# Kernel optimization log

Measured on AMD Instinct MI355X. Metric: run time of the kernel, lower is better.

Reference implementation:

```python
import jax, jax.numpy as jnp
import numpy as np

# ---- fixed sizes ----
N_IN = 100_000          # total inner nodes
NODES_PER_INNER = 50    # nodes per inner graph
N_OUT = N_IN // NODES_PER_INNER          # 2000 outer nodes (= num inner graphs)
NODES_PER_OUTER = 125   # outer nodes per outer graph
B = N_OUT // NODES_PER_OUTER             # 16 graphs in the batch
DEG = 8
E_IN = N_IN * DEG        # 800_000 inner edges
E_OUT = N_OUT * DEG      # 16_000 outer edges
IN_FEATS = 64
OUT_FEATS = 64
H = 128                  # h_feats = [128]*6
NUM_CLASSES = 10


def _rand_edges(key, n_graphs, nodes_per_graph, edges_per_graph):
    """Random edges that stay inside each graph of a batched graph."""
    k1, k2 = jax.random.split(key)
    src_l = jax.random.randint(k1, (n_graphs, edges_per_graph), 0, nodes_per_graph)
    dst_l = jax.random.randint(k2, (n_graphs, edges_per_graph), 0, nodes_per_graph)
    off = (jnp.arange(n_graphs) * nodes_per_graph)[:, None]
    return ((src_l + off).reshape(-1).astype(jnp.int32),
            (dst_l + off).reshape(-1).astype(jnp.int32))


def setup_inputs() -> dict:
    key = jax.random.key(0)
    ks = jax.random.split(key, 24)
    inner_src, inner_dst = _rand_edges(ks[0], N_OUT, NODES_PER_INNER, E_IN // N_OUT)
    outer_src, outer_dst = _rand_edges(ks[1], B, NODES_PER_OUTER, E_OUT // B)

    def w(k, fan_in, fan_out):
        return jax.random.normal(k, (fan_in, fan_out), jnp.float32) * (1.0 / np.sqrt(fan_in))

    inp = {
        "in_layer_feat": jax.random.normal(ks[2], (N_IN, IN_FEATS), jnp.float32),
        "out_layer_feat": jax.random.normal(ks[3], (N_OUT, OUT_FEATS), jnp.float32),
        "inner_ew": jax.random.uniform(ks[4], (E_IN,), jnp.float32) + 0.5,
        "outer_ew": jax.random.uniform(ks[5], (E_OUT,), jnp.float32) + 0.5,
        "W1": w(ks[6], IN_FEATS, H),        "b1": jnp.zeros((H,), jnp.float32),
        "W2": w(ks[7], H, H),               "b2": jnp.zeros((H,), jnp.float32),
        "W3": w(ks[8], OUT_FEATS + H, H),   "b3": jnp.zeros((H,), jnp.float32),
        "W4": w(ks[9], H, H),               "b4": jnp.zeros((H,), jnp.float32),
        "W5": w(ks[10], H, H),              "b5": jnp.zeros((H,), jnp.float32),
        "W6": w(ks[11], H, H),              "b6": jnp.zeros((H,), jnp.float32),
        "Wc": w(ks[12], H, NUM_CLASSES),    "bc": jnp.zeros((NUM_CLASSES,), jnp.float32),
        "inner_src": inner_src, "inner_dst": inner_dst,
        "outer_src": outer_src, "outer_dst": outer_dst,
        "inner_node_graph": (jnp.arange(N_IN) // NODES_PER_INNER).astype(jnp.int32),
        "outer_node_graph": (jnp.arange(N_OUT) // NODES_PER_OUTER).astype(jnp.int32),
    }
    return inp


def graph_conv(src, dst, ew, x, W, b, n_nodes):
    """DGL GraphConv, norm='both', weighted aggregation, zero-in-degree allowed."""
    ones = jnp.ones(src.shape[0], x.dtype)
    deg_out = jnp.clip(jax.ops.segment_sum(ones, src, num_segments=n_nodes), 1.0)
    deg_in = jnp.clip(jax.ops.segment_sum(ones, dst, num_segments=n_nodes), 1.0)
    xs = x * jax.lax.rsqrt(deg_out)[:, None]                      # src normalization
    msg = xs[src] * ew[:, None]                                   # u_mul_e
    agg = jax.ops.segment_sum(msg, dst, num_segments=n_nodes)     # copy_e -> sum
    agg = agg * jax.lax.rsqrt(deg_in)[:, None]                    # dst normalization
    return agg @ W + b


def mean_nodes(h, node_graph, n_graphs, nodes_per_graph):
    return jax.ops.segment_sum(h, node_graph, num_segments=n_graphs) / nodes_per_graph


def reference(in_layer_feat, out_layer_feat, inner_ew, outer_ew,
              W1, b1, W2, b2, W3, b3, W4, b4, W5, b5, W6, b6, Wc, bc,
              inner_src, inner_dst, outer_src, outer_dst,
              inner_node_graph, outer_node_graph):
    # inner-graph message passing
    h = jax.nn.relu(graph_conv(inner_src, inner_dst, inner_ew, in_layer_feat, W1, b1, N_IN))
    h = jax.nn.relu(graph_conv(inner_src, inner_dst, inner_ew, h, W2, b2, N_IN))
    reduced = mean_nodes(h, inner_node_graph, N_OUT, float(NODES_PER_INNER))  # [N_OUT, H]
    merged = jnp.concatenate([out_layer_feat, reduced], axis=-1)              # [N_OUT, OUT_FEATS+H]
    # outer-graph message passing
    h = jax.nn.relu(graph_conv(outer_src, outer_dst, outer_ew, merged, W3, b3, N_OUT))
    h = jax.nn.relu(graph_conv(outer_src, outer_dst, outer_ew, h, W4, b4, N_OUT))
    h = jax.nn.relu(graph_conv(outer_src, outer_dst, outer_ew, h, W5, b5, N_OUT))
    h = jax.nn.relu(graph_conv(outer_src, outer_dst, outer_ew, h, W6, b6, N_OUT))
    hg = mean_nodes(h, outer_node_graph, B, float(NODES_PER_OUTER))           # [B, H]
    return hg @ Wc + bc                                                       # [B, NUM_CLASSES]
```

## Files before the change

kernel.cpp:

```cpp
#include <hip/hip_runtime.h>

#define NPI 50
#define EPI 400
#define NPO 125
#define EPO 1000
#define N_IN 100000
#define N_OUT 2000
#define NB 16
#define NC 10

typedef _Float16 half_t;
typedef _Float16 f16x8 __attribute__((ext_vector_type(8)));
typedef float f32x4 __attribute__((ext_vector_type(4)));

#define MFMA(a, b, c) __builtin_amdgcn_mfma_f32_16x16x32_f16(a, b, c, 0, 0, 0)

__device__ __forceinline__ f16x8 lds_ld8(const half_t* base, int row, int k, int strideB) {
    return *(const f16x8*)((const char*)base + row * strideB + ((k * 2) ^ ((row & 7) << 4)));
}
__device__ __forceinline__ void lds_st1(half_t* base, int row, int col, int strideB, float v) {
    *(half_t*)((char*)base + row * strideB + ((col * 2) ^ ((row & 7) << 4))) = (half_t)v;
}
__device__ __forceinline__ void lds_st1h(half_t* base, int row, int col, int strideB, half_t v) {
    *(half_t*)((char*)base + row * strideB + ((col * 2) ^ ((row & 7) << 4))) = v;
}
__device__ __forceinline__ void lds_st8(half_t* base, int row, int k, int strideB, f16x8 v) {
    *(f16x8*)((char*)base + row * strideB + ((k * 2) ^ ((row & 7) << 4))) = v;
}
__device__ __forceinline__ f16x8 scr_ld8(const half_t* base, int row, int k) {
    return *(const f16x8*)((const char*)base + row * 64 + ((k * 2) ^ ((row & 3) << 4)));
}
__device__ __forceinline__ void scr_st1(half_t* base, int row, int col, float v) {
    *(half_t*)((char*)base + row * 64 + ((col * 2) ^ ((row & 3) << 4))) = (half_t)v;
}

__global__ __launch_bounds__(256) void k_pre(
    const float* __restrict__ W1, const float* __restrict__ W2,
    const float* __restrict__ W3, const float* __restrict__ W4,
    const float* __restrict__ W5, const float* __restrict__ W6,
    half_t* __restrict__ WT1, half_t* __restrict__ WT2,
    half_t* __restrict__ WT3, half_t* __restrict__ WT4,
    half_t* __restrict__ WT5, half_t* __restrict__ WT6,
    const float* __restrict__ ew, const int* __restrict__ esrc,
    const int* __restrict__ edst, half_t* __restrict__ Aout)
{
    __shared__ float Af[NPO * NPO];
    __shared__ int cO[NPO], cI[NPO];
    __shared__ float rso[NPO], rsi[NPO];
    const int t = threadIdx.x;

    if (blockIdx.x < 384) {
        int i = blockIdx.x * 256 + t;
        const float* src; half_t* dst; int K;
        if      (i < 8192)  { src = W1; dst = WT1; K = 64; }
        else if (i < 24576) { src = W2; dst = WT2; K = 128; i -= 8192; }
        else if (i < 49152) { src = W3; dst = WT3; K = 192; i -= 24576; }
        else if (i < 65536) { src = W4; dst = WT4; K = 128; i -= 49152; }
        else if (i < 81920) { src = W5; dst = WT5; K = 128; i -= 65536; }
        else                { src = W6; dst = WT6; K = 128; i -= 81920; }
        int c = i & 127, k = i >> 7;
        dst[c * K + k] = (half_t)src[k * 128 + c];
        return;
    }

    const int g = blockIdx.x - 384;
    const int nb = g * NPO, eb = g * EPO;
    for (int i = t; i < NPO * NPO; i += 256) Af[i] = 0.f;
    if (t < NPO) { cO[t] = 0; cI[t] = 0; }
    __syncthreads();
    for (int e = t; e < EPO; e += 256) {
        int s = esrc[eb + e] - nb, d = edst[eb + e] - nb;
        atomicAdd(&Af[d * NPO + s], ew[eb + e]);
        atomicAdd(&cO[s], 1); atomicAdd(&cI[d], 1);
    }
    __syncthreads();
    if (t < NPO) {
        rso[t] = rsqrtf((float)max(cO[t], 1));
        rsi[t] = rsqrtf((float)max(cI[t], 1));
    }
    __syncthreads();
    for (int i = t; i < 128 * 16; i += 256) {
        int d = i >> 4, s0 = (i & 15) * 8;
        f16x8 v;
        #pragma unroll
        for (int j = 0; j < 8; j++) {
            int s = s0 + j;
            float x = (d < NPO && s < NPO) ? Af[d * NPO + s] * rsi[d] * rso[s] : 0.f;
            v[j] = (half_t)x;
        }
        *(f16x8*)&Aout[(size_t)g * 16384 + d * 128 + s0] = v;
    }
}

__global__ __launch_bounds__(256, 7) void k_inner(
    const float* __restrict__ X, const float* __restrict__ outfeat,
    const float* __restrict__ ew, const int* __restrict__ esrc,
    const int* __restrict__ edst,
    const half_t* __restrict__ WT1, const float* __restrict__ b1,
    const half_t* __restrict__ WT2, const float* __restrict__ b2,
    half_t* __restrict__ merged)
{
    __shared__ alignas(16) char smem[21504];
    half_t* R2  = (half_t*)smem;
    float*  Af  = (float*)smem;
    half_t* scr = (half_t*)(smem + 16384);
    float*  pool= (float*)(smem + 20480);
    int*    cO  = (int*)(smem + 20992);
    int*    cI  = (int*)(smem + 21248);

    const int g = blockIdx.x, t = threadIdx.x;
    const int w = t >> 6, l = t & 63, lr = l & 15, lk = l >> 4;
    const int nb = g * NPI, eb = g * EPI;
    half_t* scrw = scr + w * 512;

    float ofv = (t < 64) ? outfeat[(size_t)g * 64 + t] : 0.f;
    int s0e, d0e; float w0e;
    { int e = eb + t; s0e = esrc[e] - nb; d0e = edst[e] - nb; w0e = ew[e]; }
    int s1e = 0, d1e = 0; float w1e = 0.f;
    const bool e1v = (t + 256 < EPI);
    if (e1v) { int e = eb + t + 256; s1e = esrc[e] - nb; d1e = edst[e] - nb; w1e = ew[e]; }
    const int srow = t >> 2, qc = t & 3;
    float4 xr0 = {0,0,0,0}, xr1 = xr0, xr2 = xr0, xr3 = xr0;
    if (srow < NPI) {
        const float* xp = &X[(size_t)(nb + srow) * 64 + qc * 16];
        xr0 = *(const float4*)(xp + 0);
        xr1 = *(const float4*)(xp + 4);
        xr2 = *(const float4*)(xp + 8);
        xr3 = *(const float4*)(xp + 12);
    }

    if (t < 64) { cO[t] = 0; cI[t] = 0; }
    if (t >= 64 && t < 192) pool[t - 64] = 0.f;
    for (int i = t; i < 4096; i += 256) Af[i] = 0.f;
    __syncthreads();

    atomicAdd(&Af[d0e * 64 + (s0e ^ ((d0e & 7) << 2))], w0e);
    atomicAdd(&cO[s0e], 1); atomicAdd(&cI[d0e], 1);
    if (e1v) {
        atomicAdd(&Af[d1e * 64 + (s1e ^ ((d1e & 7) << 2))], w1e);
        atomicAdd(&cO[s1e], 1); atomicAdd(&cI[d1e], 1);
    }
    __syncthreads();

    f16x8 afr[2];
    {
        const int r = w * 16 + lr;
        const int sw = (r & 7) << 2;
        const float rsi_l = rsqrtf((float)max(cI[r], 1));
        #pragma unroll
        for (int ks = 0; ks < 2; ks++) {
            const int c0 = ks * 32 + lk * 8;
            f32x4 v0 = *(const f32x4*)&Af[r * 64 + (c0 ^ sw)];
            f32x4 v1 = *(const f32x4*)&Af[r * 64 + ((c0 + 4) ^ sw)];
            f16x8 fr;
            #pragma unroll
            for (int j = 0; j < 4; j++)
                fr[j] = (half_t)(v0[j] * rsi_l * rsqrtf((float)max(cO[c0 + j], 1)));
            #pragma unroll
            for (int j = 0; j < 4; j++)
                fr[4 + j] = (half_t)(v1[j] * rsi_l * rsqrtf((float)max(cO[c0 + 4 + j], 1)));
            afr[ks] = fr;
        }
    }
    __syncthreads();

    {
        float xv[16] = {xr0.x,xr0.y,xr0.z,xr0.w, xr1.x,xr1.y,xr1.z,xr1.w,
                        xr2.x,xr2.y,xr2.z,xr2.w, xr3.x,xr3.y,xr3.z,xr3.w};
        #pragma unroll
        for (int i = 0; i < 16; i++) lds_st1(R2, qc * 16 + i, srow, 128, xv[i]);
    }
    __syncthreads();

    f32x4 hacc[8] = {};
    #pragma unroll
    for (int kf = 0; kf < 2; kf++) {
        #pragma unroll
        for (int j = 0; j < 2; j++) {
            const int ft = kf * 2 + j;
            f32x4 tacc = {};
            #pragma unroll
            for (int ks = 0; ks < 2; ks++) {
                f16x8 b = lds_ld8(R2, ft * 16 + lr, ks * 32 + lk * 8, 128);
                tacc = MFMA(afr[ks], b, tacc);
            }
            #pragma unroll
            for (int q = 0; q < 4; q++) scr_st1(scrw, lk * 4 + q, j * 16 + lr, tacc[q]);
        }
        f16x8 a1 = scr_ld8(scrw, lr, lk * 8);
        #pragma unroll
        for (int nt = 0; nt < 8; nt++) {
            f16x8 b = *(const f16x8*)&WT1[(nt * 16 + lr) * 64 + kf * 32 + lk * 8];
            hacc[nt] = MFMA(a1, b, hacc[nt]);
        }
    }
    __syncthreads();
    #pragma unroll
    for (int nt = 0; nt < 8; nt++) {
        int c = nt * 16 + lr;
        float bb = b1[c];
        #pragma unroll
        for (int q = 0; q < 4; q++)
            lds_st1(R2, c, w * 16 + lk * 4 + q, 128, fmaxf(hacc[nt][q] + bb, 0.f));
    }
    __syncthreads();

    f32x4 h2[8] = {};
    #pragma unroll
    for (int kf = 0; kf < 4; kf++) {
        #pragma unroll
        for (int j = 0; j < 2; j++) {
            const int ft = kf * 2 + j;
            f32x4 tacc = {};
            #pragma unroll
            for (int ks = 0; ks < 2; ks++) {
                f16x8 b = lds_ld8(R2, ft * 16 + lr, ks * 32 + lk * 8, 128);
                tacc = MFMA(afr[ks], b, tacc);
            }
            #pragma unroll
            for (int q = 0; q < 4; q++) scr_st1(scrw, lk * 4 + q, j * 16 + lr, tacc[q]);
        }
        f16x8 a1 = scr_ld8(scrw, lr, lk * 8);
        #pragma unroll
        for (int nt = 0; nt < 8; nt++) {
            f16x8 b = *(const f16x8*)&WT2[(nt * 16 + lr) * 128 + kf * 32 + lk * 8];
            h2[nt] = MFMA(a1, b, h2[nt]);
        }
    }
    #pragma unroll
    for (int nt = 0; nt < 8; nt++) {
        int c = nt * 16 + lr;
        float bb = b2[c];
        float ps = 0.f;
        #pragma unroll
        for (int q = 0; q < 4; q++) {
            int m = w * 16 + lk * 4 + q;
            float v = fmaxf(h2[nt][q] + bb, 0.f);
            ps += (m < NPI) ? v : 0.f;
        }
        ps += __shfl_xor(ps, 16);
        ps += __shfl_xor(ps, 32);
        if (lk == 0) atomicAdd(&pool[c], ps);
    }
    __syncthreads();
    if (t < 64) merged[(size_t)g * 192 + t] = (half_t)ofv;
    else if (t < 192) merged[(size_t)g * 192 + t] = (half_t)(pool[t - 64] * (1.f / NPI));
}

template <int FIN, bool STAGE, bool LAST>
__device__ __forceinline__ void outer_layer(
    const half_t* AgL, const half_t* __restrict__ mg,
    const half_t* __restrict__ WT, const float* __restrict__ bias,
    half_t* bufP, half_t* bufQ, float* pool,
    int w, int lr, int lk, int t)
{
    f32x4 hacc[8] = {};
    constexpr int NCH = FIN / 64;
    #pragma unroll
    for (int ch = 0; ch < NCH; ch++) {
        if constexpr (STAGE) {
            __syncthreads();
            for (int i = t; i < 1024; i += 512) {
                int s = i >> 3, fo = (i & 7) * 8;
                f16x8 hv = {};
                if (s < NPO) hv = *(const f16x8*)&mg[(size_t)s * 192 + ch * 64 + fo];
                #pragma unroll
                for (int j = 0; j < 8; j++) lds_st1h(bufP, fo + j, s, 256, hv[j]);
            }
            __syncthreads();
        }
        const int rb = STAGE ? 0 : ch * 64;
        f32x4 tacc[4] = {};
        #pragma unroll
        for (int ks = 0; ks < 4; ks++) {
            f16x8 a = lds_ld8(AgL, w * 16 + lr, ks * 32 + lk * 8, 256);
            #pragma unroll
            for (int nt = 0; nt < 4; nt++) {
                f16x8 b = lds_ld8(bufP, rb + nt * 16 + lr, ks * 32 + lk * 8, 256);
                tacc[nt] = MFMA(a, b, tacc[nt]);
            }
        }
        #pragma unroll
        for (int nt = 0; nt < 4; nt++)
            #pragma unroll
            for (int q = 0; q < 4; q++)
                lds_st1(bufQ, w * 16 + lk * 4 + q, nt * 16 + lr, 128, tacc[nt][q]);
        #pragma unroll
        for (int ks2 = 0; ks2 < 2; ks2++) {
            f16x8 a1 = lds_ld8(bufQ, w * 16 + lr, ks2 * 32 + lk * 8, 128);
            #pragma unroll
            for (int nt = 0; nt < 8; nt++) {
                f16x8 b = *(const f16x8*)&WT[(nt * 16 + lr) * FIN + ch * 64 + ks2 * 32 + lk * 8];
                hacc[nt] = MFMA(a1, b, hacc[nt]);
            }
        }
    }
    __syncthreads();
    if constexpr (!LAST) {
        #pragma unroll
        for (int nt = 0; nt < 8; nt++) {
            int c = nt * 16 + lr;
            float bb = bias[c];
            #pragma unroll
            for (int q = 0; q < 4; q++)
                lds_st1(bufP, c, w * 16 + lk * 4 + q, 256, fmaxf(hacc[nt][q] + bb, 0.f));
        }
        __syncthreads();
    } else {
        #pragma unroll
        for (int nt = 0; nt < 8; nt++) {
            int c = nt * 16 + lr;
            float bb = bias[c];
            float ps = 0.f;
            #pragma unroll
            for (int q = 0; q < 4; q++) {
                int d = w * 16 + lk * 4 + q;
                float v = fmaxf(hacc[nt][q] + bb, 0.f);
                ps += (d < NPO) ? v : 0.f;
            }
            ps += __shfl_xor(ps, 16);
            ps += __shfl_xor(ps, 32);
            if (lk == 0) atomicAdd(&pool[c], ps);
        }
        __syncthreads();
    }
}

__global__ __launch_bounds__(512) void k_outer(
    const half_t* __restrict__ Aout, const half_t* __restrict__ merged,
    const half_t* __restrict__ WT3, const float* __restrict__ b3,
    const half_t* __restrict__ WT4, const float* __restrict__ b4,
    const half_t* __restrict__ WT5, const float* __restrict__ b5,
    const half_t* __restrict__ WT6, const float* __restrict__ b6,
    const float* __restrict__ Wc, const float* __restrict__ bc,
    float* __restrict__ out)
{
    __shared__ alignas(16) char smem[82432];
    half_t* AgL  = (half_t*)smem;
    half_t* bufP = (half_t*)(smem + 32768);
    half_t* bufQ = (half_t*)(smem + 65536);
    float*  pool = (float*)(smem + 81920);

    const int g = blockIdx.x, t = threadIdx.x;
    const int w = t >> 6, l = t & 63, lr = l & 15, lk = l >> 4;
    const half_t* mg = merged + (size_t)g * NPO * 192;

    for (int i = t; i < 2048; i += 512) {
        int row = i >> 4, k0 = (i & 15) * 8;
        f16x8 v = *(const f16x8*)&Aout[(size_t)g * 16384 + row * 128 + k0];
        lds_st8(AgL, row, k0, 256, v);
    }
    if (t < 128) pool[t] = 0.f;
    __syncthreads();

    outer_layer<192, true,  false>(AgL, mg, WT3, b3, bufP, bufQ, pool, w, lr, lk, t);
    outer_layer<128, false, false>(AgL, nullptr, WT4, b4, bufP, bufQ, pool, w, lr, lk, t);
    outer_layer<128, false, false>(AgL, nullptr, WT5, b5, bufP, bufQ, pool, w, lr, lk, t);
    outer_layer<128, false, true >(AgL, nullptr, WT6, b6, bufP, bufQ, pool, w, lr, lk, t);

    if (t < NC) {
        float acc = bc[t];
        for (int k = 0; k < 128; k++)
            acc = fmaf(pool[k] * (1.f / NPO), Wc[k * NC + t], acc);
        out[g * NC + t] = acc;
    }
}

extern "C" void kernel_launch(void* const* d_in, const int* in_sizes, int n_in,
                              void* d_out, int out_size, void* d_ws, size_t ws_size,
                              hipStream_t stream)
{
    const float* X       = (const float*)d_in[0];
    const float* outfeat = (const float*)d_in[1];
    const float* iew     = (const float*)d_in[2];
    const float* oew     = (const float*)d_in[3];
    const float* W1 = (const float*)d_in[4];  const float* b1 = (const float*)d_in[5];
    const float* W2 = (const float*)d_in[6];  const float* b2 = (const float*)d_in[7];
    const float* W3 = (const float*)d_in[8];  const float* b3 = (const float*)d_in[9];
    const float* W4 = (const float*)d_in[10]; const float* b4 = (const float*)d_in[11];
    const float* W5 = (const float*)d_in[12]; const float* b5 = (const float*)d_in[13];
    const float* W6 = (const float*)d_in[14]; const float* b6 = (const float*)d_in[15];
    const float* Wc = (const float*)d_in[16]; const float* bc = (const float*)d_in[17];
    const int* isrc = (const int*)d_in[18];   const int* idst = (const int*)d_in[19];
    const int* osrc = (const int*)d_in[20];   const int* odst = (const int*)d_in[21];

    char* base = (char*)d_ws;
    half_t* WT1 = (half_t*)(base + 0);
    half_t* WT2 = (half_t*)(base + 16384);
    half_t* WT3 = (half_t*)(base + 49152);
    half_t* WT4 = (half_t*)(base + 98304);
    half_t* WT5 = (half_t*)(base + 131072);
    half_t* WT6 = (half_t*)(base + 163840);
    half_t* AoutG  = (half_t*)(base + 196608);
    half_t* merged = (half_t*)(base + 720896);

    k_pre<<<400, 256, 0, stream>>>(W1, W2, W3, W4, W5, W6,
                                   WT1, WT2, WT3, WT4, WT5, WT6,
                                   oew, osrc, odst, AoutG);
    k_inner<<<N_OUT, 256, 0, stream>>>(X, outfeat, iew, isrc, idst,
                                       WT1, b1, WT2, b2, merged);
    k_outer<<<NB, 512, 0, stream>>>(AoutG, merged, WT3, b3, WT4, b4,
                                    WT5, b5, WT6, b6, Wc, bc, (float*)d_out);
}
```

Baseline: 141.4 us.

## Build outer normalized adjacency inside k_outer and pack inner features to half early

The outer-graph adjacency build and degree normalization move out of k_pre into k_outer. The adjacency now lives in LDS space that is later reused for the layer buffers, so the global Aout buffer is no longer written and read back, and k_pre shrinks to a weight transpose. k_inner converts its input feature rows to fp16 as soon as they are loaded, which keeps fewer registers live before the LDS store. Its occupancy hint drops from 7 to 5 blocks. The trade-off is that the atomic-heavy adjacency build now runs serially on only 16 blocks in the final kernel, and k_outer needs more LDS.

```diff
diff --git a/kernel.cpp b/kernel.cpp
--- a/kernel.cpp
+++ b/kernel.cpp
@@ -40,59 +40,21 @@
     const float* __restrict__ W5, const float* __restrict__ W6,
     half_t* __restrict__ WT1, half_t* __restrict__ WT2,
     half_t* __restrict__ WT3, half_t* __restrict__ WT4,
-    half_t* __restrict__ WT5, half_t* __restrict__ WT6,
-    const float* __restrict__ ew, const int* __restrict__ esrc,
-    const int* __restrict__ edst, half_t* __restrict__ Aout)
-{
-    __shared__ float Af[NPO * NPO];
-    __shared__ int cO[NPO], cI[NPO];
-    __shared__ float rso[NPO], rsi[NPO];
-    const int t = threadIdx.x;
-
-    if (blockIdx.x < 384) {
-        int i = blockIdx.x * 256 + t;
-        const float* src; half_t* dst; int K;
-        if      (i < 8192)  { src = W1; dst = WT1; K = 64; }
-        else if (i < 24576) { src = W2; dst = WT2; K = 128; i -= 8192; }
-        else if (i < 49152) { src = W3; dst = WT3; K = 192; i -= 24576; }
-        else if (i < 65536) { src = W4; dst = WT4; K = 128; i -= 49152; }
-        else if (i < 81920) { src = W5; dst = WT5; K = 128; i -= 65536; }
-        else                { src = W6; dst = WT6; K = 128; i -= 81920; }
-        int c = i & 127, k = i >> 7;
-        dst[c * K + k] = (half_t)src[k * 128 + c];
-        return;
-    }
-
-    const int g = blockIdx.x - 384;
-    const int nb = g * NPO, eb = g * EPO;
-    for (int i = t; i < NPO * NPO; i += 256) Af[i] = 0.f;
-    if (t < NPO) { cO[t] = 0; cI[t] = 0; }
-    __syncthreads();
-    for (int e = t; e < EPO; e += 256) {
-        int s = esrc[eb + e] - nb, d = edst[eb + e] - nb;
-        atomicAdd(&Af[d * NPO + s], ew[eb + e]);
-        atomicAdd(&cO[s], 1); atomicAdd(&cI[d], 1);
-    }
-    __syncthreads();
-    if (t < NPO) {
-        rso[t] = rsqrtf((float)max(cO[t], 1));
-        rsi[t] = rsqrtf((float)max(cI[t], 1));
-    }
-    __syncthreads();
-    for (int i = t; i < 128 * 16; i += 256) {
-        int d = i >> 4, s0 = (i & 15) * 8;
-        f16x8 v;
-        #pragma unroll
-        for (int j = 0; j < 8; j++) {
-            int s = s0 + j;
-            float x = (d < NPO && s < NPO) ? Af[d * NPO + s] * rsi[d] * rso[s] : 0.f;
-            v[j] = (half_t)x;
-        }
-        *(f16x8*)&Aout[(size_t)g * 16384 + d * 128 + s0] = v;
-    }
-}
-
-__global__ __launch_bounds__(256, 7) void k_inner(
+    half_t* __restrict__ WT5, half_t* __restrict__ WT6)
+{
+    int i = blockIdx.x * 256 + threadIdx.x;
+    const float* src; half_t* dst; int K;
+    if      (i < 8192)  { src = W1; dst = WT1; K = 64; }
+    else if (i < 24576) { src = W2; dst = WT2; K = 128; i -= 8192; }
+    else if (i < 49152) { src = W3; dst = WT3; K = 192; i -= 24576; }
+    else if (i < 65536) { src = W4; dst = WT4; K = 128; i -= 49152; }
+    else if (i < 81920) { src = W5; dst = WT5; K = 128; i -= 65536; }
+    else                { src = W6; dst = WT6; K = 128; i -= 81920; }
+    int c = i & 127, k = i >> 7;
+    dst[c * K + k] = (half_t)src[k * 128 + c];
+}
+
+__global__ __launch_bounds__(256, 5) void k_inner(
     const float* __restrict__ X, const float* __restrict__ outfeat,
     const float* __restrict__ ew, const int* __restrict__ esrc,
     const int* __restrict__ edst,
@@ -120,13 +82,15 @@
     const bool e1v = (t + 256 < EPI);
     if (e1v) { int e = eb + t + 256; s1e = esrc[e] - nb; d1e = edst[e] - nb; w1e = ew[e]; }
     const int srow = t >> 2, qc = t & 3;
-    float4 xr0 = {0,0,0,0}, xr1 = xr0, xr2 = xr0, xr3 = xr0;
+    f16x8 xh0 = {}, xh1 = {};
     if (srow < NPI) {
         const float* xp = &X[(size_t)(nb + srow) * 64 + qc * 16];
-        xr0 = *(const float4*)(xp + 0);
-        xr1 = *(const float4*)(xp + 4);
-        xr2 = *(const float4*)(xp + 8);
-        xr3 = *(const float4*)(xp + 12);
+        float4 a = *(const float4*)(xp + 0), b = *(const float4*)(xp + 4);
+        float4 c = *(const float4*)(xp + 8), d = *(const float4*)(xp + 12);
+        xh0[0]=(half_t)a.x; xh0[1]=(half_t)a.y; xh0[2]=(half_t)a.z; xh0[3]=(half_t)a.w;
+        xh0[4]=(half_t)b.x; xh0[5]=(half_t)b.y; xh0[6]=(half_t)b.z; xh0[7]=(half_t)b.w;
+        xh1[0]=(half_t)c.x; xh1[1]=(half_t)c.y; xh1[2]=(half_t)c.z; xh1[3]=(half_t)c.w;
+        xh1[4]=(half_t)d.x; xh1[5]=(half_t)d.y; xh1[6]=(half_t)d.z; xh1[7]=(half_t)d.w;
     }
 
     if (t < 64) { cO[t] = 0; cI[t] = 0; }
@@ -164,12 +128,10 @@
     }
     __syncthreads();
 
-    {
-        float xv[16] = {xr0.x,xr0.y,xr0.z,xr0.w, xr1.x,xr1.y,xr1.z,xr1.w,
-                        xr2.x,xr2.y,xr2.z,xr2.w, xr3.x,xr3.y,xr3.z,xr3.w};
-        #pragma unroll
-        for (int i = 0; i < 16; i++) lds_st1(R2, qc * 16 + i, srow, 128, xv[i]);
-    }
+    #pragma unroll
+    for (int i = 0; i < 8; i++) lds_st1h(R2, qc * 16 + i, srow, 128, xh0[i]);
+    #pragma unroll
+    for (int i = 0; i < 8; i++) lds_st1h(R2, qc * 16 + 8 + i, srow, 128, xh1[i]);
     __syncthreads();
 
     f32x4 hacc[8] = {};
@@ -327,7 +289,8 @@
 }
 
 __global__ __launch_bounds__(512) void k_outer(
-    const half_t* __restrict__ Aout, const half_t* __restrict__ merged,
+    const float* __restrict__ ewo, const int* __restrict__ esrc,
+    const int* __restrict__ edst, const half_t* __restrict__ merged,
     const half_t* __restrict__ WT3, const float* __restrict__ b3,
     const half_t* __restrict__ WT4, const float* __restrict__ b4,
     const half_t* __restrict__ WT5, const float* __restrict__ b5,
@@ -335,22 +298,43 @@
     const float* __restrict__ Wc, const float* __restrict__ bc,
     float* __restrict__ out)
 {
-    __shared__ alignas(16) char smem[82432];
+    __shared__ alignas(16) char smem[98304];
     half_t* AgL  = (half_t*)smem;
+    float*  Af   = (float*)(smem + 32768);
     half_t* bufP = (half_t*)(smem + 32768);
     half_t* bufQ = (half_t*)(smem + 65536);
-    float*  pool = (float*)(smem + 81920);
+    float*  pool = (float*)(smem + 95280);
+    int*    cO   = (int*)(smem + 95792);
+    int*    cI   = (int*)(smem + 96292);
 
     const int g = blockIdx.x, t = threadIdx.x;
     const int w = t >> 6, l = t & 63, lr = l & 15, lk = l >> 4;
+    const int nb = g * NPO, eb = g * EPO;
     const half_t* mg = merged + (size_t)g * NPO * 192;
 
+    for (int i = t; i < NPO * NPO; i += 512) Af[i] = 0.f;
+    if (t < NPO) { cO[t] = 0; cI[t] = 0; }
+    if (t >= 128 && t < 256) pool[t - 128] = 0.f;
+    __syncthreads();
+    for (int e = t; e < EPO; e += 512) {
+        int s = esrc[eb + e] - nb, d = edst[eb + e] - nb;
+        atomicAdd(&Af[d * NPO + s], ewo[eb + e]);
+        atomicAdd(&cO[s], 1); atomicAdd(&cI[d], 1);
+    }
+    __syncthreads();
     for (int i = t; i < 2048; i += 512) {
         int row = i >> 4, k0 = (i & 15) * 8;
-        f16x8 v = *(const f16x8*)&Aout[(size_t)g * 16384 + row * 128 + k0];
+        const float rsi_l = (row < NPO) ? rsqrtf((float)max(cI[row], 1)) : 0.f;
+        f16x8 v;
+        #pragma unroll
+        for (int j = 0; j < 8; j++) {
+            int s = k0 + j;
+            float x = (row < NPO && s < NPO)
+                ? Af[row * NPO + s] * rsi_l * rsqrtf((float)max(cO[s], 1)) : 0.f;
+            v[j] = (half_t)x;
+        }
         lds_st8(AgL, row, k0, 256, v);
     }
-    if (t < 128) pool[t] = 0.f;
     __syncthreads();
 
     outer_layer<192, true,  false>(AgL, mg, WT3, b3, bufP, bufQ, pool, w, lr, lk, t);
@@ -391,14 +375,12 @@
     half_t* WT4 = (half_t*)(base + 98304);
     half_t* WT5 = (half_t*)(base + 131072);
     half_t* WT6 = (half_t*)(base + 163840);
-    half_t* AoutG  = (half_t*)(base + 196608);
-    half_t* merged = (half_t*)(base + 720896);
-
-    k_pre<<<400, 256, 0, stream>>>(W1, W2, W3, W4, W5, W6,
-                                   WT1, WT2, WT3, WT4, WT5, WT6,
-                                   oew, osrc, odst, AoutG);
+    half_t* merged = (half_t*)(base + 196608);
+
+    k_pre<<<384, 256, 0, stream>>>(W1, W2, W3, W4, W5, W6,
+                                   WT1, WT2, WT3, WT4, WT5, WT6);
     k_inner<<<N_OUT, 256, 0, stream>>>(X, outfeat, iew, isrc, idst,
                                        WT1, b1, WT2, b2, merged);
-    k_outer<<<NB, 512, 0, stream>>>(AoutG, merged, WT3, b3, WT4, b4,
+    k_outer<<<NB, 512, 0, stream>>>(oew, osrc, odst, merged, WT3, b3, WT4, b4,
                                     WT5, b5, WT6, b6, Wc, bc, (float*)d_out);
 }
```

Result: faster. 128.5 us (-9.1%).
